# Kernel optimization log

Hardware: AMD Instinct MI355X
Metric: run time of the kernel (lower is better)

The kernel has to match this reference:

```python
import jax, jax.numpy as jnp
import numpy as np

HIDDEN = 2048
HEADS = 16
HEAD_DIM = HIDDEN // HEADS  # 128
B, S = 2, 2048


def setup_inputs() -> dict:
    key = jax.random.key(0)
    ks = jax.random.split(key, 9)
    s_in = 1.0 / np.sqrt(HIDDEN)
    return {
        "X": jax.random.normal(ks[0], (B, S, HIDDEN), dtype=jnp.float32),
        "attention_mask": jnp.ones((B, S, S), dtype=jnp.int32),
        "Wq": jax.random.uniform(ks[1], (HIDDEN, HIDDEN), jnp.float32, -s_in, s_in),
        "bq": jax.random.uniform(ks[2], (HIDDEN,), jnp.float32, -s_in, s_in),
        "Wk": jax.random.uniform(ks[3], (HIDDEN, HEAD_DIM), jnp.float32, -s_in, s_in),
        "bk": jax.random.uniform(ks[4], (HEAD_DIM,), jnp.float32, -s_in, s_in),
        "Wv": jax.random.uniform(ks[5], (HIDDEN, HEAD_DIM), jnp.float32, -s_in, s_in),
        "bv": jax.random.uniform(ks[6], (HEAD_DIM,), jnp.float32, -s_in, s_in),
        "Wo": jax.random.uniform(ks[7], (HIDDEN, HIDDEN), jnp.float32, -s_in, s_in),
        "bo": jax.random.uniform(ks[8], (HIDDEN,), jnp.float32, -s_in, s_in),
    }


def reference(X, attention_mask, Wq, bq, Wk, bk, Wv, bv, Wo, bo):
    b, s, _ = X.shape
    # Projections
    Q = X @ Wq + bq                      # (B, S, H*D)
    K = X @ Wk + bk                      # (B, S, D)  shared across heads (MQA)
    V = X @ Wv + bv                      # (B, S, D)
    Q = Q.reshape(b, s, HEADS, HEAD_DIM).transpose(0, 2, 1, 3)  # (B, H, S, D)
    scale = 1.0 / jnp.sqrt(jnp.float32(HEAD_DIM))
    # QK^T with shared K head
    scores = jnp.einsum('bhqd,bkd->bhqk', Q, K) * scale          # (B, H, S, S)
    scores = jnp.where(attention_mask[:, None, :, :] == 0, -jnp.inf, scores)
    attn = jax.nn.softmax(scores, axis=-1)
    # dropout_rate = 0.0 (eval) -> identity
    out = jnp.einsum('bhqk,bkd->bhqd', attn, V)                  # (B, H, S, D)
    out = out.transpose(0, 2, 1, 3).reshape(b, s, HIDDEN)        # (B, S, hidden)
    return out @ Wo + bo
```

## Files before the change

kernel.cpp:

```cpp
#include <hip/hip_runtime.h>
#include <cstdint>
#include <cstddef>

#define HIDDEN 2048
#define HEADS 16
#define HD 128
#define BSZ 2
#define SEQ 2048
#define MTOT (BSZ * SEQ)
#define NQKV (HIDDEN + 2 * HD)
#define SL2E 0.12751743f

typedef unsigned short ushort_t;
typedef __attribute__((ext_vector_type(8))) __bf16 bf16x8;
typedef __attribute__((ext_vector_type(4))) float f32x4;
typedef __attribute__((ext_vector_type(16))) float f32x16;

typedef __attribute__((address_space(3))) unsigned int as3_u32;
typedef __attribute__((address_space(1))) const unsigned int as1_u32;

__device__ __forceinline__ ushort_t f2bf(float x) {
  union { float f; unsigned u; } v; v.f = x;
  unsigned r = v.u + 0x7fffu + ((v.u >> 16) & 1u);
  return (ushort_t)(r >> 16);
}
__device__ __forceinline__ unsigned pk_bf16(float a, float b) {
  union { float f; unsigned u; } x, y; x.f = a; y.f = b;
  return (x.u >> 16) | (y.u & 0xFFFF0000u);
}

__device__ __forceinline__ void gld16(const void* g, void* lds) {
  __builtin_amdgcn_global_load_lds((as1_u32*)g, (as3_u32*)lds, 16, 0, 0);
}

__device__ __forceinline__ void barf() {
  asm volatile("" ::: "memory");
  __builtin_amdgcn_s_barrier();
  asm volatile("" ::: "memory");
}

__global__ __launch_bounds__(256) void cvt_bf16_kernel(
    const float* __restrict__ in, ushort_t* __restrict__ out, int n4) {
  int i = blockIdx.x * 256 + threadIdx.x;
  if (i >= n4) return;
  float4 v = ((const float4*)in)[i];
  ushort4 o;
  o.x = f2bf(v.x); o.y = f2bf(v.y); o.z = f2bf(v.z); o.w = f2bf(v.w);
  ((ushort4*)out)[i] = o;
}

__global__ __launch_bounds__(256) void cvtT_qkv_kernel(
    const float* __restrict__ Wq, const float* __restrict__ Wk,
    const float* __restrict__ Wv, ushort_t* __restrict__ WT) {
  __shared__ float tile[32][36];
  const int t = threadIdx.x;
  const int nb = blockIdx.x * 32, kb = blockIdx.y * 32;
  const float* W; int N, nc; float scale;
  if (nb < HIDDEN)            { W = Wq; N = HIDDEN; nc = nb;               scale = SL2E; }
  else if (nb < HIDDEN + HD)  { W = Wk; N = HD;     nc = nb - HIDDEN;      scale = 1.f; }
  else                        { W = Wv; N = HD;     nc = nb - HIDDEN - HD; scale = 1.f; }
  {
    int row = t >> 3, c4 = (t & 7) << 2;
    float4 v = *(const float4*)(W + (size_t)(kb + row) * N + nc + c4);
    tile[row][c4] = v.x * scale; tile[row][c4 + 1] = v.y * scale;
    tile[row][c4 + 2] = v.z * scale; tile[row][c4 + 3] = v.w * scale;
  }
  __syncthreads();
  {
    int nl = t >> 3, k4 = (t & 7) << 2;
    ushort4 o;
    o.x = f2bf(tile[k4 + 0][nl]); o.y = f2bf(tile[k4 + 1][nl]);
    o.z = f2bf(tile[k4 + 2][nl]); o.w = f2bf(tile[k4 + 3][nl]);
    *(ushort4*)(WT + (size_t)(nb + nl) * HIDDEN + kb + k4) = o;
  }
}

__global__ __launch_bounds__(256) void cvtT_kernel(
    const float* __restrict__ W, ushort_t* __restrict__ WT, int K, int N) {
  __shared__ float tile[32][36];
  const int t = threadIdx.x;
  const int kb = blockIdx.y * 32, nb = blockIdx.x * 32;
  {
    int row = t >> 3, c4 = (t & 7) << 2;
    float4 v = *(const float4*)(W + (size_t)(kb + row) * N + nb + c4);
    tile[row][c4] = v.x; tile[row][c4 + 1] = v.y;
    tile[row][c4 + 2] = v.z; tile[row][c4 + 3] = v.w;
  }
  __syncthreads();
  {
    int nl = t >> 3, k4 = (t & 7) << 2;
    ushort4 o;
    o.x = f2bf(tile[k4 + 0][nl]); o.y = f2bf(tile[k4 + 1][nl]);
    o.z = f2bf(tile[k4 + 2][nl]); o.w = f2bf(tile[k4 + 3][nl]);
    *(ushort4*)(WT + (size_t)(nb + nl) * K + kb + k4) = o;
  }
}

__global__ __launch_bounds__(256) void transpose_v_kernel(
    const ushort_t* __restrict__ Vin, ushort_t* __restrict__ Vt) {
  __shared__ ushort_t tile[32][40];
  const int t = threadIdx.x;
  const int rb = blockIdx.x * 32, cb = blockIdx.y * 32;
  {
    int row = t >> 3, c4 = (t & 7) << 2;
    ushort4 v = *(const ushort4*)(Vin + (size_t)(rb + row) * NQKV + cb + c4);
    tile[row][c4] = v.x; tile[row][c4 + 1] = v.y;
    tile[row][c4 + 2] = v.z; tile[row][c4 + 3] = v.w;
  }
  __syncthreads();
  {
    int dl = t >> 3, r4 = (t & 7) << 2;
    ushort4 o;
    o.x = tile[r4 + 0][dl]; o.y = tile[r4 + 1][dl];
    o.z = tile[r4 + 2][dl]; o.w = tile[r4 + 3][dl];
    *(ushort4*)(Vt + (size_t)(cb + dl) * MTOT + rb + r4) = o;
  }
}

__global__ void concat_bias_kernel(const float* __restrict__ bq,
                                   const float* __restrict__ bk,
                                   const float* __restrict__ bv,
                                   float* __restrict__ o) {
  int i = blockIdx.x * 256 + threadIdx.x;
  if (i >= NQKV) return;
  o[i] = (i < HIDDEN) ? bq[i] * SL2E
       : (i < HIDDEN + HD ? bk[i - HIDDEN] : bv[i - HIDDEN - HD]);
}

__global__ __launch_bounds__(256) void mask_flags_kernel(
    const int* __restrict__ mask, int* __restrict__ flags) {
  const int kt = blockIdx.x, qt = blockIdx.y, b = blockIdx.z;
  const int t = threadIdx.x;
  int allv = 1, anyv = 0;
  const size_t base = (size_t)b * SEQ * SEQ + (size_t)qt * 128 * SEQ + kt * 64;
  for (int i = t; i < 2048; i += 256) {
    const int row = i >> 4, c4 = (i & 15) << 2;
    const int4 v = *(const int4*)(mask + base + (size_t)row * SEQ + c4);
    const int nz = (v.x != 0) & (v.y != 0) & (v.z != 0) & (v.w != 0);
    const int nzany = (v.x != 0) | (v.y != 0) | (v.z != 0) | (v.w != 0);
    allv &= nz; anyv |= nzany;
  }
  const int wAll = __all(allv), wAny = __any(anyv);
  __shared__ int sA[4], sO[4];
  if ((t & 63) == 0) { sA[t >> 6] = wAll; sO[t >> 6] = wAny; }
  __syncthreads();
  if (t == 0) {
    const int A = sA[0] & sA[1] & sA[2] & sA[3];
    const int O = sO[0] | sO[1] | sO[2] | sO[3];
    flags[(b * 16 + qt) * 32 + kt] = A ? 2 : (O ? 1 : 0);
  }
}

template <int OUTF32>
__global__ __launch_bounds__(512, 1) void gemm_mfma8(
    const ushort_t* __restrict__ A, const ushort_t* __restrict__ Bt,
    const float* __restrict__ bias, void* __restrict__ C,
    int M, int N, int K, int nm_per_xcd) {
  __shared__ ushort_t As[2][256 * 64];
  __shared__ ushort_t Bs[2][256 * 64];
  const int t = threadIdx.x;
  const int w = t >> 6, l = t & 63;
  const int id = blockIdx.x;
  const int xcd = id & 7, jb = id >> 3;
  const int mt = xcd * nm_per_xcd + (jb % nm_per_xcd);
  const int nt = jb / nm_per_xcd;
  const int mb = mt * 256, nb = nt * 256;
  const int wm = (w >> 2) * 128, wn = (w & 3) * 64;
  const int fl = l & 15, g = l >> 4;
  const int srow = l >> 3;
  const int clog = (l & 7) ^ (srow & 7);
  const int ntile = K >> 6;

  auto stageA = [&](int s, int half, int kt) {
    const int rr = half * 128 + w * 16;
    for (int jj = 0; jj < 2; ++jj)
      gld16(A + (size_t)(mb + rr + jj * 8 + srow) * K + kt * 64 + clog * 8,
            &As[s][(rr + jj * 8) * 64]);
  };
  auto stageB = [&](int s, int half, int kt) {
    const int rr = half * 128 + w * 16;
    for (int jj = 0; jj < 2; ++jj)
      gld16(Bt + (size_t)(nb + rr + jj * 8 + srow) * K + kt * 64 + clog * 8,
            &Bs[s][(rr + jj * 8) * 64]);
  };

  f32x4 acc[8][4];
#pragma unroll
  for (int i = 0; i < 8; ++i)
#pragma unroll
    for (int jf = 0; jf < 4; ++jf) acc[i][jf] = (f32x4){0.f, 0.f, 0.f, 0.f};

  stageB(0, 0, 0); stageB(0, 1, 0);
  stageA(0, 0, 0); stageA(0, 1, 0);
  stageB(1, 0, 1); stageB(1, 1, 1);
  asm volatile("s_waitcnt vmcnt(4)" ::: "memory");
  barf();

  for (int it = 0; it < ntile / 2; ++it) {
    const int kb2 = 2 * it + 1;
    int kc = 2 * it + 2; if (kc >= ntile) kc = ntile - 1;
    int kd = 2 * it + 3; if (kd >= ntile) kd = ntile - 1;

    bf16x8 af[4][2], b0[2][2], b1[2][2];

#pragma unroll
    for (int h = 0; h < 2; ++h) {
      const ushort_t* Ac = As[h];
      const ushort_t* Bc = Bs[h];

#pragma unroll
      for (int i = 0; i < 4; ++i) {
        const int m = wm + i * 16 + fl;
#pragma unroll
        for (int s2 = 0; s2 < 2; ++s2)
          af[i][s2] =
              *(const bf16x8*)&Ac[m * 64 + (((s2 << 2) + g) ^ (fl & 7)) * 8];
      }
#pragma unroll
      for (int jf = 0; jf < 2; ++jf) {
        const int n = wn + jf * 16 + fl;
#pragma unroll
        for (int s2 = 0; s2 < 2; ++s2)
          b0[jf][s2] =
              *(const bf16x8*)&Bc[n * 64 + (((s2 << 2) + g) ^ (fl & 7)) * 8];
      }
      if (h == 0) stageA(1, 0, kb2); else stageA(0, 0, kc);
      barf();
      asm volatile("s_waitcnt lgkmcnt(0)" ::: "memory");
      __builtin_amdgcn_sched_barrier(0);
      __builtin_amdgcn_s_setprio(1);
#pragma unroll
      for (int i = 0; i < 4; ++i)
#pragma unroll
        for (int jf = 0; jf < 2; ++jf)
#pragma unroll
          for (int s2 = 0; s2 < 2; ++s2)
            acc[i][jf] = __builtin_amdgcn_mfma_f32_16x16x32_bf16(
                af[i][s2], b0[jf][s2], acc[i][jf], 0, 0, 0);
      __builtin_amdgcn_s_setprio(0);
      barf();

#pragma unroll
      for (int jf = 0; jf < 2; ++jf) {
        const int n = wn + (2 + jf) * 16 + fl;
#pragma unroll
        for (int s2 = 0; s2 < 2; ++s2)
          b1[jf][s2] =
              *(const bf16x8*)&Bc[n * 64 + (((s2 << 2) + g) ^ (fl & 7)) * 8];
      }
      if (h == 0) stageA(1, 1, kb2); else stageA(0, 1, kc);
      barf();
      asm volatile("s_waitcnt lgkmcnt(0)" ::: "memory");
      __builtin_amdgcn_sched_barrier(0);
      __builtin_amdgcn_s_setprio(1);
#pragma unroll
      for (int i = 0; i < 4; ++i)
#pragma unroll
        for (int jf = 0; jf < 2; ++jf)
#pragma unroll
          for (int s2 = 0; s2 < 2; ++s2)
            acc[i][2 + jf] = __builtin_amdgcn_mfma_f32_16x16x32_bf16(
                af[i][s2], b1[jf][s2], acc[i][2 + jf], 0, 0, 0);
      __builtin_amdgcn_s_setprio(0);
      barf();

#pragma unroll
      for (int i = 0; i < 4; ++i) {
        const int m = wm + (4 + i) * 16 + fl;
#pragma unroll
        for (int s2 = 0; s2 < 2; ++s2)
          af[i][s2] =
              *(const bf16x8*)&Ac[m * 64 + (((s2 << 2) + g) ^ (fl & 7)) * 8];
      }
      if (h == 0) stageB(0, 0, kc); else stageB(1, 0, kd);
      barf();
      asm volatile("s_waitcnt lgkmcnt(0)" ::: "memory");
      __builtin_amdgcn_sched_barrier(0);
      __builtin_amdgcn_s_setprio(1);
#pragma unroll
      for (int i = 0; i < 4; ++i)
#pragma unroll
        for (int jf = 0; jf < 2; ++jf)
#pragma unroll
          for (int s2 = 0; s2 < 2; ++s2)
            acc[4 + i][2 + jf] = __builtin_amdgcn_mfma_f32_16x16x32_bf16(
                af[i][s2], b1[jf][s2], acc[4 + i][2 + jf], 0, 0, 0);
      __builtin_amdgcn_s_setprio(0);
      barf();

      if (h == 0) stageB(0, 1, kc); else stageB(1, 1, kd);
      asm volatile("s_waitcnt vmcnt(4)" ::: "memory");
      barf();
      __builtin_amdgcn_s_setprio(1);
#pragma unroll
      for (int i = 0; i < 4; ++i)
#pragma unroll
        for (int jf = 0; jf < 2; ++jf)
#pragma unroll
          for (int s2 = 0; s2 < 2; ++s2)
            acc[4 + i][jf] = __builtin_amdgcn_mfma_f32_16x16x32_bf16(
                af[i][s2], b0[jf][s2], acc[4 + i][jf], 0, 0, 0);
      __builtin_amdgcn_s_setprio(0);
      barf();
    }
  }

#pragma unroll
  for (int jf = 0; jf < 4; ++jf) {
    const int col = nb + wn + jf * 16 + fl;
    const float bv = bias[col];
#pragma unroll
    for (int i = 0; i < 8; ++i) {
      const int row0 = mb + wm + i * 16 + g * 4;
#pragma unroll
      for (int r = 0; r < 4; ++r) {
        const float val = acc[i][jf][r] + bv;
        if (OUTF32)
          ((float*)C)[(size_t)(row0 + r) * N + col] = val;
        else
          ((ushort_t*)C)[(size_t)(row0 + r) * N + col] = f2bf(val);
      }
    }
  }
}

__global__ __launch_bounds__(256, 2) void flash_mfma(
    const ushort_t* __restrict__ QKV,
    const ushort_t* __restrict__ Vt,
    const int* __restrict__ mask,
    const int* __restrict__ flags,
    ushort_t* __restrict__ Ab)
{
  __shared__ ushort_t Kbuf[2][64 * 128];
  __shared__ ushort_t Vbuf[2][64 * 128];

  const int qt = blockIdx.x, h = blockIdx.y, b = blockIdx.z;
  const int t = threadIdx.x, w = t >> 6, l = t & 63;
  const int q31 = l & 31, hi = l >> 5;
  const int qbase = qt * 128;
  const int qrow = qbase + w * 32 + q31;

  bf16x8 qf[8];
#pragma unroll
  for (int ks = 0; ks < 8; ++ks)
    qf[ks] = *(const bf16x8*)(QKV + (size_t)(b * SEQ + qrow) * NQKV + h * HD +
                              ks * 16 + hi * 8);

  bf16x8 onesf;
  {
    const ushort_t ov = (q31 == 0) ? (ushort_t)0x3F80 : (ushort_t)0;
#pragma unroll
    for (int jj = 0; jj < 8; ++jj) ((ushort_t*)&onesf)[jj] = ov;
  }

#pragma unroll
  for (int j = 0; j < 4; ++j) {
    const int inst = w * 4 + j;
    const int krow = inst * 4 + (l >> 4);
    const int ck = (l & 15) ^ (krow & 15);
    gld16(QKV + (size_t)(b * SEQ + krow) * NQKV + HIDDEN + ck * 8,
          &Kbuf[0][inst * 512]);
    const int vr = inst * 4 + (l >> 4);
    const int clog = (l & 15) ^ (vr & 15);
    const int d = 2 * vr + (clog >> 3);
    gld16(Vt + (size_t)d * MTOT + b * SEQ + (clog & 7) * 8,
          &Vbuf[0][inst * 512]);
  }

  const size_t mbase = (size_t)b * SEQ * SEQ;

  f32x16 oacc[4], lacc;
#pragma unroll
  for (int d = 0; d < 4; ++d)
#pragma unroll
    for (int r = 0; r < 16; ++r) oacc[d][r] = 0.f;
#pragma unroll
  for (int r = 0; r < 16; ++r) lacc[r] = 0.f;

  int cur = 0;
  for (int kt = 0; kt < SEQ / 64; ++kt) {
    const int kbase = kt * 64;
    const int flag = flags[((b * 16 + qt) << 5) + kt];
    __syncthreads();

    {
      const int knb = (kt + 1 < SEQ / 64) ? (kbase + 64) : kbase;
#pragma unroll
      for (int j = 0; j < 4; ++j) {
        const int inst = w * 4 + j;
        const int krow = inst * 4 + (l >> 4);
        const int ck = (l & 15) ^ (krow & 15);
        gld16(QKV + (size_t)(b * SEQ + knb + krow) * NQKV + HIDDEN + ck * 8,
              &Kbuf[cur ^ 1][inst * 512]);
        const int vr = inst * 4 + (l >> 4);
        const int clog = (l & 15) ^ (vr & 15);
        const int d = 2 * vr + (clog >> 3);
        gld16(Vt + (size_t)d * MTOT + b * SEQ + knb + (clog & 7) * 8,
              &Vbuf[cur ^ 1][inst * 512]);
      }
    }

    const ushort_t* Kc = &Kbuf[cur][0];
    f32x16 sc[2];
#pragma unroll
    for (int kk = 0; kk < 2; ++kk)
#pragma unroll
      for (int r = 0; r < 16; ++r) sc[kk][r] = 0.f;

    __builtin_amdgcn_s_setprio(1);
#pragma unroll
    for (int ks = 0; ks < 8; ++ks)
#pragma unroll
      for (int kk = 0; kk < 2; ++kk) {
        const int key = kk * 32 + q31;
        const bf16x8 kf = *(const bf16x8*)&Kc[key * 128 +
                                              (((ks << 1) + hi) ^ (key & 15)) * 8];
        sc[kk] = __builtin_amdgcn_mfma_f32_32x32x16_bf16(kf, qf[ks], sc[kk],
                                                         0, 0, 0);
      }
    __builtin_amdgcn_s_setprio(0);

    if (flag != 2) {
#pragma unroll
      for (int kk = 0; kk < 2; ++kk)
#pragma unroll
        for (int r = 0; r < 16; ++r) {
          const int key = kbase + kk * 32 + (r & 3) + ((r >> 2) << 3) + (hi << 2);
          if (!mask[mbase + (size_t)qrow * SEQ + key]) sc[kk][r] = -1e30f;
        }
    }

    bf16x8 pa[4];
#pragma unroll
    for (int kk = 0; kk < 2; ++kk) {
      float pv[16];
#pragma unroll
      for (int r = 0; r < 16; ++r) pv[r] = __builtin_amdgcn_exp2f(sc[kk][r]);
#pragma unroll
      for (int half = 0; half < 2; ++half) {
        const int bs = half * 8;
        unsigned a0 = pk_bf16(pv[bs + 0], pv[bs + 1]);
        unsigned a1 = pk_bf16(pv[bs + 2], pv[bs + 3]);
        unsigned b0 = pk_bf16(pv[bs + 4], pv[bs + 5]);
        unsigned b1 = pk_bf16(pv[bs + 6], pv[bs + 7]);
        asm("v_permlane32_swap_b32 %0, %1" : "+v"(a0), "+v"(b0));
        asm("v_permlane32_swap_b32 %0, %1" : "+v"(a1), "+v"(b1));
        union { unsigned u[4]; bf16x8 v; } uu;
        uu.u[0] = a0; uu.u[1] = a1; uu.u[2] = b0; uu.u[3] = b1;
        pa[kk * 2 + half] = uu.v;
      }
    }

    const ushort_t* Vc = &Vbuf[cur][0];
    __builtin_amdgcn_s_setprio(1);
#pragma unroll
    for (int ks = 0; ks < 4; ++ks) {
#pragma unroll
      for (int dt = 0; dt < 4; ++dt) {
        const int d = dt * 32 + q31;
        const int vr = d >> 1;
        const int clog = ((d & 1) << 3) + (ks << 1) + hi;
        const bf16x8 vf =
            *(const bf16x8*)&Vc[vr * 128 + (clog ^ (vr & 15)) * 8];
        oacc[dt] = __builtin_amdgcn_mfma_f32_32x32x16_bf16(pa[ks], vf,
                                                           oacc[dt], 0, 0, 0);
      }
      lacc = __builtin_amdgcn_mfma_f32_32x32x16_bf16(pa[ks], onesf, lacc,
                                                     0, 0, 0);
    }
    __builtin_amdgcn_s_setprio(0);
    cur ^= 1;
  }

#pragma unroll
  for (int r = 0; r < 16; ++r) {
    const float ls = __shfl(lacc[r], l & 32, 64);
    const float invl = 1.0f / ls;
    const int row = b * SEQ + qbase + w * 32 + (r & 3) + ((r >> 2) << 3) +
                    (hi << 2);
#pragma unroll
    for (int dt = 0; dt < 4; ++dt)
      Ab[(size_t)row * HIDDEN + h * HD + dt * 32 + q31] =
          f2bf(oacc[dt][r] * invl);
  }
}

extern "C" void kernel_launch(void* const* d_in, const int* in_sizes, int n_in,
                              void* d_out, int out_size, void* d_ws, size_t ws_size,
                              hipStream_t stream) {
  const float* X  = (const float*)d_in[0];
  const int* mask = (const int*)d_in[1];
  const float* Wq = (const float*)d_in[2];
  const float* bq = (const float*)d_in[3];
  const float* Wk = (const float*)d_in[4];
  const float* bk = (const float*)d_in[5];
  const float* Wv = (const float*)d_in[6];
  const float* bv = (const float*)d_in[7];
  const float* Wo = (const float*)d_in[8];
  const float* bo = (const float*)d_in[9];
  float* out = (float*)d_out;

  char* p = (char*)d_ws;
  ushort_t* QKVb = (ushort_t*)p; p += (size_t)MTOT * NQKV * 2;
  ushort_t* Xb   = (ushort_t*)p; p += (size_t)MTOT * HIDDEN * 2;
  ushort_t* WT   = (ushort_t*)p; p += (size_t)NQKV * HIDDEN * 2;
  ushort_t* WoT  = (ushort_t*)p; p += (size_t)HIDDEN * HIDDEN * 2;
  ushort_t* Vt   = (ushort_t*)p; p += (size_t)HD * MTOT * 2;
  float* biasQKV = (float*)p;    p += 4096;
  int* flags     = (int*)p;      p += BSZ * 16 * 32 * 4;
  ushort_t* Ab = Xb;

  cvt_bf16_kernel<<<(MTOT * HIDDEN / 4 + 255) / 256, 256, 0, stream>>>(
      X, Xb, MTOT * HIDDEN / 4);
  cvtT_qkv_kernel<<<dim3(NQKV / 32, HIDDEN / 32), 256, 0, stream>>>(
      Wq, Wk, Wv, WT);
  cvtT_kernel<<<dim3(HIDDEN / 32, HIDDEN / 32), 256, 0, stream>>>(
      Wo, WoT, HIDDEN, HIDDEN);
  concat_bias_kernel<<<(NQKV + 255) / 256, 256, 0, stream>>>(bq, bk, bv, biasQKV);
  mask_flags_kernel<<<dim3(32, 16, BSZ), 256, 0, stream>>>(mask, flags);

  gemm_mfma8<0><<<dim3((MTOT / 256) * (NQKV / 256)), 512, 0, stream>>>(
      Xb, WT, biasQKV, QKVb, MTOT, NQKV, HIDDEN, (MTOT / 256) / 8);
  transpose_v_kernel<<<dim3(MTOT / 32, HD / 32), 256, 0, stream>>>(
      QKVb + HIDDEN + HD, Vt);
  flash_mfma<<<dim3(SEQ / 128, HEADS, BSZ), 256, 0, stream>>>(
      QKVb, Vt, mask, flags, Ab);
  gemm_mfma8<1><<<dim3((MTOT / 256) * (HIDDEN / 256)), 512, 0, stream>>>(
      Ab, WoT, bo, out, MTOT, HIDDEN, HIDDEN, (MTOT / 256) / 8);
}
```

Measured before the change: 349.2 us.

## Merge prep kernels, fuse V transpose into QKV GEMM epilogue, restage loads

Folds the five preprocessing kernels (X convert, weight transposes, bias concat, mask flags) into one launch that dispatches on block index. Drops the separate V transpose kernel by having the QKV GEMM epilogue also write the V columns transposed into Vt. The GEMM prefetch schedule changes from staggered A/B half-tile loads spread across the sub-steps to one bulk stageAll per half-iteration, with the vmcnt wait raised to 8. This removes launch overhead and a pass over V, at the cost of uncoalesced scattered writes to Vt and possibly less overlap of loads with MFMA work.

```diff
diff --git a/kernel.cpp b/kernel.cpp
--- a/kernel.cpp
+++ b/kernel.cpp
@@ -39,123 +39,116 @@
   asm volatile("" ::: "memory");
 }
 
-__global__ __launch_bounds__(256) void cvt_bf16_kernel(
-    const float* __restrict__ in, ushort_t* __restrict__ out, int n4) {
-  int i = blockIdx.x * 256 + threadIdx.x;
-  if (i >= n4) return;
-  float4 v = ((const float4*)in)[i];
-  ushort4 o;
-  o.x = f2bf(v.x); o.y = f2bf(v.y); o.z = f2bf(v.z); o.w = f2bf(v.w);
-  ((ushort4*)out)[i] = o;
-}
-
-__global__ __launch_bounds__(256) void cvtT_qkv_kernel(
+#define PREP_NM (32 * 16 * BSZ)
+#define PREP_N0 (MTOT * HIDDEN / 4 / 256)
+#define PREP_N1 ((NQKV / 32) * (HIDDEN / 32))
+#define PREP_N2 ((HIDDEN / 32) * (HIDDEN / 32))
+#define PREP_N4 ((NQKV + 255) / 256)
+#define PREP_NB (PREP_NM + PREP_N0 + PREP_N1 + PREP_N2 + PREP_N4)
+
+__global__ __launch_bounds__(256) void prep_kernel(
+    const float* __restrict__ X, ushort_t* __restrict__ Xb,
     const float* __restrict__ Wq, const float* __restrict__ Wk,
-    const float* __restrict__ Wv, ushort_t* __restrict__ WT) {
-  __shared__ float tile[32][36];
+    const float* __restrict__ Wv, ushort_t* __restrict__ WT,
+    const float* __restrict__ Wo, ushort_t* __restrict__ WoT,
+    const int* __restrict__ mask, int* __restrict__ flags,
+    const float* __restrict__ bq, const float* __restrict__ bk,
+    const float* __restrict__ bv, float* __restrict__ biasQKV) {
+  __shared__ float tileF[32][36];
+  __shared__ int sAO[8];
   const int t = threadIdx.x;
-  const int nb = blockIdx.x * 32, kb = blockIdx.y * 32;
-  const float* W; int N, nc; float scale;
-  if (nb < HIDDEN)            { W = Wq; N = HIDDEN; nc = nb;               scale = SL2E; }
-  else if (nb < HIDDEN + HD)  { W = Wk; N = HD;     nc = nb - HIDDEN;      scale = 1.f; }
-  else                        { W = Wv; N = HD;     nc = nb - HIDDEN - HD; scale = 1.f; }
+  int j = blockIdx.x;
+
+  if (j < PREP_NM) {
+    const int kt = j & 31, qt = (j >> 5) & 15, b = j >> 9;
+    int allv = 1, anyv = 0;
+    const size_t base = (size_t)b * SEQ * SEQ + (size_t)qt * 128 * SEQ + kt * 64;
+    for (int i = t; i < 2048; i += 256) {
+      const int row = i >> 4, c4 = (i & 15) << 2;
+      const int4 v = *(const int4*)(mask + base + (size_t)row * SEQ + c4);
+      const int nz = (v.x != 0) & (v.y != 0) & (v.z != 0) & (v.w != 0);
+      const int nzany = (v.x != 0) | (v.y != 0) | (v.z != 0) | (v.w != 0);
+      allv &= nz; anyv |= nzany;
+    }
+    const int wAll = __all(allv), wAny = __any(anyv);
+    if ((t & 63) == 0) { sAO[t >> 6] = wAll; sAO[4 + (t >> 6)] = wAny; }
+    __syncthreads();
+    if (t == 0) {
+      const int A = sAO[0] & sAO[1] & sAO[2] & sAO[3];
+      const int O = sAO[4] | sAO[5] | sAO[6] | sAO[7];
+      flags[(b * 16 + qt) * 32 + kt] = A ? 2 : (O ? 1 : 0);
+    }
+    return;
+  }
+  j -= PREP_NM;
+
+  if (j < PREP_N0) {
+    const int i = j * 256 + t;
+    float4 v = ((const float4*)X)[i];
+    ushort4 o;
+    o.x = f2bf(v.x); o.y = f2bf(v.y); o.z = f2bf(v.z); o.w = f2bf(v.w);
+    ((ushort4*)Xb)[i] = o;
+    return;
+  }
+  j -= PREP_N0;
+
+  if (j < PREP_N1) {
+    const int nb = (j % (NQKV / 32)) * 32, kb = (j / (NQKV / 32)) * 32;
+    const float* W; int N, nc; float scale;
+    if (nb < HIDDEN)           { W = Wq; N = HIDDEN; nc = nb;               scale = SL2E; }
+    else if (nb < HIDDEN + HD) { W = Wk; N = HD;     nc = nb - HIDDEN;      scale = 1.f; }
+    else                       { W = Wv; N = HD;     nc = nb - HIDDEN - HD; scale = 1.f; }
+    {
+      int row = t >> 3, c4 = (t & 7) << 2;
+      float4 v = *(const float4*)(W + (size_t)(kb + row) * N + nc + c4);
+      tileF[row][c4] = v.x * scale; tileF[row][c4 + 1] = v.y * scale;
+      tileF[row][c4 + 2] = v.z * scale; tileF[row][c4 + 3] = v.w * scale;
+    }
+    __syncthreads();
+    {
+      int nl = t >> 3, k4 = (t & 7) << 2;
+      ushort4 o;
+      o.x = f2bf(tileF[k4 + 0][nl]); o.y = f2bf(tileF[k4 + 1][nl]);
+      o.z = f2bf(tileF[k4 + 2][nl]); o.w = f2bf(tileF[k4 + 3][nl]);
+      *(ushort4*)(WT + (size_t)(nb + nl) * HIDDEN + kb + k4) = o;
+    }
+    return;
+  }
+  j -= PREP_N1;
+
+  if (j < PREP_N2) {
+    const int nb = (j % (HIDDEN / 32)) * 32, kb = (j / (HIDDEN / 32)) * 32;
+    {
+      int row = t >> 3, c4 = (t & 7) << 2;
+      float4 v = *(const float4*)(Wo + (size_t)(kb + row) * HIDDEN + nb + c4);
+      tileF[row][c4] = v.x; tileF[row][c4 + 1] = v.y;
+      tileF[row][c4 + 2] = v.z; tileF[row][c4 + 3] = v.w;
+    }
+    __syncthreads();
+    {
+      int nl = t >> 3, k4 = (t & 7) << 2;
+      ushort4 o;
+      o.x = f2bf(tileF[k4 + 0][nl]); o.y = f2bf(tileF[k4 + 1][nl]);
+      o.z = f2bf(tileF[k4 + 2][nl]); o.w = f2bf(tileF[k4 + 3][nl]);
+      *(ushort4*)(WoT + (size_t)(nb + nl) * HIDDEN + kb + k4) = o;
+    }
+    return;
+  }
+  j -= PREP_N2;
+
   {
-    int row = t >> 3, c4 = (t & 7) << 2;
-    float4 v = *(const float4*)(W + (size_t)(kb + row) * N + nc + c4);
-    tile[row][c4] = v.x * scale; tile[row][c4 + 1] = v.y * scale;
-    tile[row][c4 + 2] = v.z * scale; tile[row][c4 + 3] = v.w * scale;
-  }
-  __syncthreads();
-  {
-    int nl = t >> 3, k4 = (t & 7) << 2;
-    ushort4 o;
-    o.x = f2bf(tile[k4 + 0][nl]); o.y = f2bf(tile[k4 + 1][nl]);
-    o.z = f2bf(tile[k4 + 2][nl]); o.w = f2bf(tile[k4 + 3][nl]);
-    *(ushort4*)(WT + (size_t)(nb + nl) * HIDDEN + kb + k4) = o;
-  }
-}
-
-__global__ __launch_bounds__(256) void cvtT_kernel(
-    const float* __restrict__ W, ushort_t* __restrict__ WT, int K, int N) {
-  __shared__ float tile[32][36];
-  const int t = threadIdx.x;
-  const int kb = blockIdx.y * 32, nb = blockIdx.x * 32;
-  {
-    int row = t >> 3, c4 = (t & 7) << 2;
-    float4 v = *(const float4*)(W + (size_t)(kb + row) * N + nb + c4);
-    tile[row][c4] = v.x; tile[row][c4 + 1] = v.y;
-    tile[row][c4 + 2] = v.z; tile[row][c4 + 3] = v.w;
-  }
-  __syncthreads();
-  {
-    int nl = t >> 3, k4 = (t & 7) << 2;
-    ushort4 o;
-    o.x = f2bf(tile[k4 + 0][nl]); o.y = f2bf(tile[k4 + 1][nl]);
-    o.z = f2bf(tile[k4 + 2][nl]); o.w = f2bf(tile[k4 + 3][nl]);
-    *(ushort4*)(WT + (size_t)(nb + nl) * K + kb + k4) = o;
-  }
-}
-
-__global__ __launch_bounds__(256) void transpose_v_kernel(
-    const ushort_t* __restrict__ Vin, ushort_t* __restrict__ Vt) {
-  __shared__ ushort_t tile[32][40];
-  const int t = threadIdx.x;
-  const int rb = blockIdx.x * 32, cb = blockIdx.y * 32;
-  {
-    int row = t >> 3, c4 = (t & 7) << 2;
-    ushort4 v = *(const ushort4*)(Vin + (size_t)(rb + row) * NQKV + cb + c4);
-    tile[row][c4] = v.x; tile[row][c4 + 1] = v.y;
-    tile[row][c4 + 2] = v.z; tile[row][c4 + 3] = v.w;
-  }
-  __syncthreads();
-  {
-    int dl = t >> 3, r4 = (t & 7) << 2;
-    ushort4 o;
-    o.x = tile[r4 + 0][dl]; o.y = tile[r4 + 1][dl];
-    o.z = tile[r4 + 2][dl]; o.w = tile[r4 + 3][dl];
-    *(ushort4*)(Vt + (size_t)(cb + dl) * MTOT + rb + r4) = o;
-  }
-}
-
-__global__ void concat_bias_kernel(const float* __restrict__ bq,
-                                   const float* __restrict__ bk,
-                                   const float* __restrict__ bv,
-                                   float* __restrict__ o) {
-  int i = blockIdx.x * 256 + threadIdx.x;
-  if (i >= NQKV) return;
-  o[i] = (i < HIDDEN) ? bq[i] * SL2E
-       : (i < HIDDEN + HD ? bk[i - HIDDEN] : bv[i - HIDDEN - HD]);
-}
-
-__global__ __launch_bounds__(256) void mask_flags_kernel(
-    const int* __restrict__ mask, int* __restrict__ flags) {
-  const int kt = blockIdx.x, qt = blockIdx.y, b = blockIdx.z;
-  const int t = threadIdx.x;
-  int allv = 1, anyv = 0;
-  const size_t base = (size_t)b * SEQ * SEQ + (size_t)qt * 128 * SEQ + kt * 64;
-  for (int i = t; i < 2048; i += 256) {
-    const int row = i >> 4, c4 = (i & 15) << 2;
-    const int4 v = *(const int4*)(mask + base + (size_t)row * SEQ + c4);
-    const int nz = (v.x != 0) & (v.y != 0) & (v.z != 0) & (v.w != 0);
-    const int nzany = (v.x != 0) | (v.y != 0) | (v.z != 0) | (v.w != 0);
-    allv &= nz; anyv |= nzany;
-  }
-  const int wAll = __all(allv), wAny = __any(anyv);
-  __shared__ int sA[4], sO[4];
-  if ((t & 63) == 0) { sA[t >> 6] = wAll; sO[t >> 6] = wAny; }
-  __syncthreads();
-  if (t == 0) {
-    const int A = sA[0] & sA[1] & sA[2] & sA[3];
-    const int O = sO[0] | sO[1] | sO[2] | sO[3];
-    flags[(b * 16 + qt) * 32 + kt] = A ? 2 : (O ? 1 : 0);
-  }
-}
-
-template <int OUTF32>
+    const int i = j * 256 + t;
+    if (i < NQKV)
+      biasQKV[i] = (i < HIDDEN) ? bq[i] * SL2E
+                 : (i < HIDDEN + HD ? bk[i - HIDDEN] : bv[i - HIDDEN - HD]);
+  }
+}
+
+template <int OUTF32, int FUSEV>
 __global__ __launch_bounds__(512, 1) void gemm_mfma8(
     const ushort_t* __restrict__ A, const ushort_t* __restrict__ Bt,
     const float* __restrict__ bias, void* __restrict__ C,
-    int M, int N, int K, int nm_per_xcd) {
+    ushort_t* __restrict__ Vt, int M, int N, int K, int nm_per_xcd) {
   __shared__ ushort_t As[2][256 * 64];
   __shared__ ushort_t Bs[2][256 * 64];
   const int t = threadIdx.x;
@@ -171,18 +164,19 @@
   const int clog = (l & 7) ^ (srow & 7);
   const int ntile = K >> 6;
 
-  auto stageA = [&](int s, int half, int kt) {
-    const int rr = half * 128 + w * 16;
-    for (int jj = 0; jj < 2; ++jj)
-      gld16(A + (size_t)(mb + rr + jj * 8 + srow) * K + kt * 64 + clog * 8,
-            &As[s][(rr + jj * 8) * 64]);
+  auto stageAll = [&](int s, int kt) {
+#pragma unroll
+    for (int half = 0; half < 2; ++half) {
+      const int rr = half * 128 + w * 16;
+#pragma unroll
+      for (int jj = 0; jj < 2; ++jj) {
+        gld16(A + (size_t)(mb + rr + jj * 8 + srow) * K + kt * 64 + clog * 8,
+              &As[s][(rr + jj * 8) * 64]);
+        gld16(Bt + (size_t)(nb + rr + jj * 8 + srow) * K + kt * 64 + clog * 8,
+              &Bs[s][(rr + jj * 8) * 64]);
+      }
+    }
   };
-  auto stageB = [&](int s, int half, int kt) {
-    const int rr = half * 128 + w * 16;
-    for (int jj = 0; jj < 2; ++jj)
-      gld16(Bt + (size_t)(nb + rr + jj * 8 + srow) * K + kt * 64 + clog * 8,
-            &Bs[s][(rr + jj * 8) * 64]);
-  };
 
   f32x4 acc[8][4];
 #pragma unroll
@@ -190,14 +184,12 @@
 #pragma unroll
     for (int jf = 0; jf < 4; ++jf) acc[i][jf] = (f32x4){0.f, 0.f, 0.f, 0.f};
 
-  stageB(0, 0, 0); stageB(0, 1, 0);
-  stageA(0, 0, 0); stageA(0, 1, 0);
-  stageB(1, 0, 1); stageB(1, 1, 1);
-  asm volatile("s_waitcnt vmcnt(4)" ::: "memory");
+  stageAll(0, 0);
+  stageAll(1, 1);
+  asm volatile("s_waitcnt vmcnt(8)" ::: "memory");
   barf();
 
   for (int it = 0; it < ntile / 2; ++it) {
-    const int kb2 = 2 * it + 1;
     int kc = 2 * it + 2; if (kc >= ntile) kc = ntile - 1;
     int kd = 2 * it + 3; if (kd >= ntile) kd = ntile - 1;
 
@@ -224,7 +216,6 @@
           b0[jf][s2] =
               *(const bf16x8*)&Bc[n * 64 + (((s2 << 2) + g) ^ (fl & 7)) * 8];
       }
-      if (h == 0) stageA(1, 0, kb2); else stageA(0, 0, kc);
       barf();
       asm volatile("s_waitcnt lgkmcnt(0)" ::: "memory");
       __builtin_amdgcn_sched_barrier(0);
@@ -248,7 +239,6 @@
           b1[jf][s2] =
               *(const bf16x8*)&Bc[n * 64 + (((s2 << 2) + g) ^ (fl & 7)) * 8];
       }
-      if (h == 0) stageA(1, 1, kb2); else stageA(0, 1, kc);
       barf();
       asm volatile("s_waitcnt lgkmcnt(0)" ::: "memory");
       __builtin_amdgcn_sched_barrier(0);
@@ -272,7 +262,6 @@
           af[i][s2] =
               *(const bf16x8*)&Ac[m * 64 + (((s2 << 2) + g) ^ (fl & 7)) * 8];
       }
-      if (h == 0) stageB(0, 0, kc); else stageB(1, 0, kd);
       barf();
       asm volatile("s_waitcnt lgkmcnt(0)" ::: "memory");
       __builtin_amdgcn_sched_barrier(0);
@@ -288,8 +277,8 @@
       __builtin_amdgcn_s_setprio(0);
       barf();
 
-      if (h == 0) stageB(0, 1, kc); else stageB(1, 1, kd);
-      asm volatile("s_waitcnt vmcnt(4)" ::: "memory");
+      stageAll(h, h == 0 ? kc : kd);
+      asm volatile("s_waitcnt vmcnt(8)" ::: "memory");
       barf();
       __builtin_amdgcn_s_setprio(1);
 #pragma unroll
@@ -309,16 +298,21 @@
   for (int jf = 0; jf < 4; ++jf) {
     const int col = nb + wn + jf * 16 + fl;
     const float bv = bias[col];
+    const int dv = col - (HIDDEN + HD);
 #pragma unroll
     for (int i = 0; i < 8; ++i) {
       const int row0 = mb + wm + i * 16 + g * 4;
 #pragma unroll
       for (int r = 0; r < 4; ++r) {
         const float val = acc[i][jf][r] + bv;
-        if (OUTF32)
+        if (OUTF32) {
           ((float*)C)[(size_t)(row0 + r) * N + col] = val;
-        else
-          ((ushort_t*)C)[(size_t)(row0 + r) * N + col] = f2bf(val);
+        } else {
+          const ushort_t bb = f2bf(val);
+          ((ushort_t*)C)[(size_t)(row0 + r) * N + col] = bb;
+          if (FUSEV && dv >= 0)
+            Vt[(size_t)dv * MTOT + row0 + r] = bb;
+        }
       }
     }
   }
@@ -501,30 +495,22 @@
   float* out = (float*)d_out;
 
   char* p = (char*)d_ws;
+  int* flags     = (int*)p;      p += BSZ * 16 * 32 * 4;
+  float* biasQKV = (float*)p;    p += 16384;
   ushort_t* QKVb = (ushort_t*)p; p += (size_t)MTOT * NQKV * 2;
   ushort_t* Xb   = (ushort_t*)p; p += (size_t)MTOT * HIDDEN * 2;
   ushort_t* WT   = (ushort_t*)p; p += (size_t)NQKV * HIDDEN * 2;
   ushort_t* WoT  = (ushort_t*)p; p += (size_t)HIDDEN * HIDDEN * 2;
   ushort_t* Vt   = (ushort_t*)p; p += (size_t)HD * MTOT * 2;
-  float* biasQKV = (float*)p;    p += 4096;
-  int* flags     = (int*)p;      p += BSZ * 16 * 32 * 4;
   ushort_t* Ab = Xb;
 
-  cvt_bf16_kernel<<<(MTOT * HIDDEN / 4 + 255) / 256, 256, 0, stream>>>(
-      X, Xb, MTOT * HIDDEN / 4);
-  cvtT_qkv_kernel<<<dim3(NQKV / 32, HIDDEN / 32), 256, 0, stream>>>(
-      Wq, Wk, Wv, WT);
-  cvtT_kernel<<<dim3(HIDDEN / 32, HIDDEN / 32), 256, 0, stream>>>(
-      Wo, WoT, HIDDEN, HIDDEN);
-  concat_bias_kernel<<<(NQKV + 255) / 256, 256, 0, stream>>>(bq, bk, bv, biasQKV);
-  mask_flags_kernel<<<dim3(32, 16, BSZ), 256, 0, stream>>>(mask, flags);
-
-  gemm_mfma8<0><<<dim3((MTOT / 256) * (NQKV / 256)), 512, 0, stream>>>(
-      Xb, WT, biasQKV, QKVb, MTOT, NQKV, HIDDEN, (MTOT / 256) / 8);
-  transpose_v_kernel<<<dim3(MTOT / 32, HD / 32), 256, 0, stream>>>(
-      QKVb + HIDDEN + HD, Vt);
+  prep_kernel<<<PREP_NB, 256, 0, stream>>>(
+      X, Xb, Wq, Wk, Wv, WT, Wo, WoT, mask, flags, bq, bk, bv, biasQKV);
+
+  gemm_mfma8<0, 1><<<dim3((MTOT / 256) * (NQKV / 256)), 512, 0, stream>>>(
+      Xb, WT, biasQKV, QKVb, Vt, MTOT, NQKV, HIDDEN, (MTOT / 256) / 8);
   flash_mfma<<<dim3(SEQ / 128, HEADS, BSZ), 256, 0, stream>>>(
       QKVb, Vt, mask, flags, Ab);
-  gemm_mfma8<1><<<dim3((MTOT / 256) * (HIDDEN / 256)), 512, 0, stream>>>(
-      Ab, WoT, bo, out, MTOT, HIDDEN, HIDDEN, (MTOT / 256) / 8);
-}
+  gemm_mfma8<1, 0><<<dim3((MTOT / 256) * (HIDDEN / 256)), 512, 0, stream>>>(
+      Ab, WoT, bo, out, nullptr, MTOT, HIDDEN, HIDDEN, (MTOT / 256) / 8);
+}
```

Measured after the change: 362.8 us. 3.9% more time.
